# Performance work log

Hardware: AMD Instinct MI355X
Metric: run time of the kernel (lower is better)

Reference implementation:

```python
import jax, jax.numpy as jnp
import numpy as np

B = 512          # batch of visual features
VF_D = 4096      # visual feature dim (VGG fc7)
HID_D = 2048     # hidden dim
EMB_D = 300      # order-embedding / label-vector dim
N_LABELS = 2000  # number of GT label vectors


def setup_inputs() -> dict:
    key = jax.random.key(0)
    ks = jax.random.split(key, 4)
    vfs = jax.random.normal(ks[0], (B, VF_D), dtype=jnp.float32)
    W1 = jax.random.normal(ks[1], (VF_D, HID_D), dtype=jnp.float32) * (1.0 / np.sqrt(VF_D))
    b1 = jnp.zeros((HID_D,), dtype=jnp.float32)
    W2 = jax.random.normal(ks[2], (HID_D, EMB_D), dtype=jnp.float32) * (1.0 / np.sqrt(HID_D))
    b2 = jnp.zeros((EMB_D,), dtype=jnp.float32)
    gt_label_vecs = jax.random.normal(ks[3], (N_LABELS, EMB_D), dtype=jnp.float32)
    return {"vfs": vfs, "W1": W1, "b1": b1, "W2": W2, "b2": b2,
            "gt_label_vecs": gt_label_vecs}


def reference(vfs, W1, b1, W2, b2, gt_label_vecs):
    # hidden_layer: ReLU -> (Dropout, identity at eval) -> Linear
    vf_hidden = jnp.dot(jax.nn.relu(vfs), W1) + b1            # [B, HID_D]
    # embedding_layer: ReLU -> Linear
    vf_emb = jnp.dot(jax.nn.relu(vf_hidden), W2) + b2         # [B, EMB_D]
    # order_sim(hypers=gt_label_vecs, hypos=vf_emb):
    #   score = -|| clamp(hypo - hyper, min=0) ||^2, batched over all pairs
    diff = jax.nn.relu(vf_emb[:, None, :] - gt_label_vecs[None, :, :])  # [B, N, D]
    score_stack = -jnp.sum(diff * diff, axis=-1)              # [B, N_LABELS]
    return score_stack, vf_emb
```

## Files before the change

### kernel.cpp

```cpp
#include <hip/hip_runtime.h>

#define B_SZ   512
#define VFD    4096
#define HIDD   2048
#define EMBD   300
#define NLAB   2000
#define NPAD   320

#define G1_SPLIT 4
#define G2_SPLIT 8

typedef __attribute__((ext_vector_type(8))) short short8x;
typedef __attribute__((ext_vector_type(4))) float f32x4;
typedef __attribute__((ext_vector_type(8))) unsigned short ushort8;
typedef __attribute__((ext_vector_type(4))) unsigned short ushort4x;
typedef __attribute__((ext_vector_type(2))) _Float16 h2;

typedef const __attribute__((address_space(1))) unsigned int* gas_t;
typedef __attribute__((address_space(3))) unsigned int* las_t;

__device__ inline unsigned short f2bf(float x) {
    unsigned u = __float_as_uint(x);
    u += 0x7FFF + ((u >> 16) & 1);
    return (unsigned short)(u >> 16);
}

__device__ inline unsigned short f2hneg(float x) {
    _Float16 h = (_Float16)(-x);
    return __builtin_bit_cast(unsigned short, h);
}

__global__ __launch_bounds__(256) void prep_kernel(
    const float* __restrict__ vfs, unsigned short* __restrict__ Xb,
    const float* __restrict__ W1, unsigned short* __restrict__ W1T,
    const float* __restrict__ W2, unsigned short* __restrict__ W2T,
    const float* __restrict__ G,  unsigned short* __restrict__ Gh)
{
    __shared__ unsigned int Lds[64][34];
    const int tid = threadIdx.x;
    const int blk = blockIdx.x;

    if (blk < 1024) {
        const int i = (blk * 256 + tid) * 8;
        float4 a = *(const float4*)&vfs[i];
        float4 b = *(const float4*)&vfs[i + 4];
        ushort8 o;
        o[0] = f2bf(fmaxf(a.x, 0.f)); o[1] = f2bf(fmaxf(a.y, 0.f));
        o[2] = f2bf(fmaxf(a.z, 0.f)); o[3] = f2bf(fmaxf(a.w, 0.f));
        o[4] = f2bf(fmaxf(b.x, 0.f)); o[5] = f2bf(fmaxf(b.y, 0.f));
        o[6] = f2bf(fmaxf(b.z, 0.f)); o[7] = f2bf(fmaxf(b.w, 0.f));
        *(ushort8*)&Xb[i] = o;
        return;
    }
    if (blk >= 3232) {
        const int i = ((blk - 3232) * 256 + tid) * 8;
        if (i + 8 <= NLAB * EMBD) {
            float4 a = *(const float4*)&G[i];
            float4 b = *(const float4*)&G[i + 4];
            ushort8 o;
            o[0] = f2hneg(a.x); o[1] = f2hneg(a.y);
            o[2] = f2hneg(a.z); o[3] = f2hneg(a.w);
            o[4] = f2hneg(b.x); o[5] = f2hneg(b.y);
            o[6] = f2hneg(b.z); o[7] = f2hneg(b.w);
            *(ushort8*)&Gh[i] = o;
        }
        return;
    }

    const float* in; unsigned short* out; int N, ldK, bx, by;
    if (blk < 3072) {
        const int b = blk - 1024;
        in = W1; out = W1T; N = HIDD; ldK = VFD; bx = b & 31; by = b >> 5;
    } else {
        const int b = blk - 3072;
        in = W2; out = W2T; N = EMBD; ldK = HIDD; bx = b % 5; by = b / 5;
    }
    const int n0 = bx * 64, k0 = by * 64;

    #pragma unroll
    for (int i = 0; i < 2; ++i) {
        const int s = tid + 256 * i;
        const int kp = s >> 4, nq = s & 15;
        const int n = n0 + nq * 4;
        float4 v0 = {0.f,0.f,0.f,0.f}, v1 = {0.f,0.f,0.f,0.f};
        if (n < N) {
            v0 = *(const float4*)&in[(size_t)(k0 + 2 * kp)     * N + n];
            v1 = *(const float4*)&in[(size_t)(k0 + 2 * kp + 1) * N + n];
        }
        Lds[nq*4+0][kp] = (unsigned)f2bf(v0.x) | ((unsigned)f2bf(v1.x) << 16);
        Lds[nq*4+1][kp] = (unsigned)f2bf(v0.y) | ((unsigned)f2bf(v1.y) << 16);
        Lds[nq*4+2][kp] = (unsigned)f2bf(v0.z) | ((unsigned)f2bf(v1.z) << 16);
        Lds[nq*4+3][kp] = (unsigned)f2bf(v0.w) | ((unsigned)f2bf(v1.w) << 16);
    }
    __syncthreads();

    #pragma unroll
    for (int i = 0; i < 2; ++i) {
        const int c = tid + 256 * i;
        const int n = c >> 3, oct = c & 7;
        uint2 lo = *(uint2*)&Lds[n][oct * 4];
        uint2 hi = *(uint2*)&Lds[n][oct * 4 + 2];
        uint4 v = make_uint4(lo.x, lo.y, hi.x, hi.y);
        *(uint4*)&out[(size_t)(n0 + n) * ldK + k0 + oct * 8] = v;
    }
}

__global__ __launch_bounds__(256) void gemm1_kernel(
    const unsigned short* __restrict__ A,
    const unsigned short* __restrict__ Bt,
    float* __restrict__ Cpart)
{
    __shared__ unsigned short As[2][4096];
    __shared__ unsigned short Bs[2][8192];

    const int tid = threadIdx.x;
    const int m0 = blockIdx.y * 64, n0 = blockIdx.x * 128;
    const int kbase = blockIdx.z * (VFD / G1_SPLIT);

    const unsigned short* ga = A + (size_t)(m0 + (tid & 63)) * VFD + kbase + (tid >> 6) * 8;
    const unsigned short* gb = Bt + (size_t)(n0 + (tid & 127)) * VFD + kbase + (tid >> 7) * 8;

    const int lane = tid & 63;
    const int wave = tid >> 6;
    const int wm = (wave & 1) * 32;
    const int wn = (wave >> 1) * 64;
    const int q = lane >> 4, l15 = lane & 15;

    f32x4 acc[2][4];
    #pragma unroll
    for (int r = 0; r < 2; ++r)
        #pragma unroll
        for (int c = 0; c < 4; ++c) acc[r][c] = (f32x4){0.f,0.f,0.f,0.f};

    #pragma unroll
    for (int i = 0; i < 2; ++i)
        __builtin_amdgcn_global_load_lds((gas_t)(const void*)(ga + i * 32),
                                         (las_t)(void*)&As[0][(tid + 256 * i) * 8], 16, 0, 0);
    #pragma unroll
    for (int i = 0; i < 4; ++i)
        __builtin_amdgcn_global_load_lds((gas_t)(const void*)(gb + i * 16),
                                         (las_t)(void*)&Bs[0][(tid + 256 * i) * 8], 16, 0, 0);

    const int iters = (VFD / G1_SPLIT) / 64;
    for (int t = 0; t < iters; ++t) {
        const int cur = t & 1, nxt = cur ^ 1;
        __syncthreads();

        if (t + 1 < iters) {
            const int ko = (t + 1) * 64;
            #pragma unroll
            for (int i = 0; i < 2; ++i)
                __builtin_amdgcn_global_load_lds((gas_t)(const void*)(ga + ko + i * 32),
                                                 (las_t)(void*)&As[nxt][(tid + 256 * i) * 8], 16, 0, 0);
            #pragma unroll
            for (int i = 0; i < 4; ++i)
                __builtin_amdgcn_global_load_lds((gas_t)(const void*)(gb + ko + i * 16),
                                                 (las_t)(void*)&Bs[nxt][(tid + 256 * i) * 8], 16, 0, 0);
        }

        #pragma unroll
        for (int kk = 0; kk < 2; ++kk) {
            const int oct = kk * 4 + q;
            short8x a0 = *(short8x*)&As[cur][(oct * 64 + wm +      l15) * 8];
            short8x a1 = *(short8x*)&As[cur][(oct * 64 + wm + 16 + l15) * 8];
            #pragma unroll
            for (int c = 0; c < 4; ++c) {
                short8x b = *(short8x*)&Bs[cur][(oct * 128 + wn + c * 16 + l15) * 8];
                acc[0][c] = __builtin_amdgcn_mfma_f32_16x16x32_bf16(a0, b, acc[0][c], 0, 0, 0);
                acc[1][c] = __builtin_amdgcn_mfma_f32_16x16x32_bf16(a1, b, acc[1][c], 0, 0, 0);
            }
        }
    }

    float* Cz = Cpart + (size_t)blockIdx.z * B_SZ * HIDD;
    #pragma unroll
    for (int r = 0; r < 2; ++r) {
        #pragma unroll
        for (int g = 0; g < 4; ++g) {
            const int rr = m0 + wm + r * 16 + q * 4 + g;
            #pragma unroll
            for (int c = 0; c < 4; ++c)
                Cz[(size_t)rr * HIDD + n0 + wn + c * 16 + l15] = acc[r][c][g];
        }
    }
}

template<int LDA, int LDB, int LDC, int KCHUNK>
__global__ __launch_bounds__(256) void gemm_bf16_kernel(
    const unsigned short* __restrict__ A,
    const unsigned short* __restrict__ Bt,
    float* __restrict__ Cpart, int M)
{
    __shared__ unsigned short As[2][4096];
    __shared__ unsigned short Bs[2][4096];

    const int tid = threadIdx.x;
    const int m0 = blockIdx.y * 64, n0 = blockIdx.x * 64;
    const int kbase = blockIdx.z * KCHUNK;

    const unsigned short* ga = A  + (size_t)(m0 + (tid & 63)) * LDA + kbase + (tid >> 6) * 8;
    const unsigned short* gb = Bt + (size_t)(n0 + (tid & 63)) * LDB + kbase + (tid >> 6) * 8;

    const int lane = tid & 63;
    const int wave = tid >> 6;
    const int wm = (wave & 1) * 32;
    const int wn = (wave >> 1) * 32;
    const int q = lane >> 4, l15 = lane & 15;

    f32x4 acc00 = {0.f,0.f,0.f,0.f}, acc01 = {0.f,0.f,0.f,0.f};
    f32x4 acc10 = {0.f,0.f,0.f,0.f}, acc11 = {0.f,0.f,0.f,0.f};

    #pragma unroll
    for (int i = 0; i < 2; ++i) {
        __builtin_amdgcn_global_load_lds((gas_t)(const void*)(ga + i * 32),
                                         (las_t)(void*)&As[0][(tid + 256 * i) * 8], 16, 0, 0);
        __builtin_amdgcn_global_load_lds((gas_t)(const void*)(gb + i * 32),
                                         (las_t)(void*)&Bs[0][(tid + 256 * i) * 8], 16, 0, 0);
    }

    const int iters = KCHUNK / 64;
    for (int t = 0; t < iters; ++t) {
        const int cur = t & 1, nxt = cur ^ 1;
        __syncthreads();

        if (t + 1 < iters) {
            const int ko = (t + 1) * 64;
            #pragma unroll
            for (int i = 0; i < 2; ++i) {
                __builtin_amdgcn_global_load_lds((gas_t)(const void*)(ga + ko + i * 32),
                                                 (las_t)(void*)&As[nxt][(tid + 256 * i) * 8], 16, 0, 0);
                __builtin_amdgcn_global_load_lds((gas_t)(const void*)(gb + ko + i * 32),
                                                 (las_t)(void*)&Bs[nxt][(tid + 256 * i) * 8], 16, 0, 0);
            }
        }

        #pragma unroll
        for (int kk = 0; kk < 2; ++kk) {
            const int oct = kk * 4 + q;
            short8x a0 = *(short8x*)&As[cur][(oct * 64 + wm +      l15) * 8];
            short8x a1 = *(short8x*)&As[cur][(oct * 64 + wm + 16 + l15) * 8];
            short8x b0 = *(short8x*)&Bs[cur][(oct * 64 + wn +      l15) * 8];
            short8x b1 = *(short8x*)&Bs[cur][(oct * 64 + wn + 16 + l15) * 8];
            acc00 = __builtin_amdgcn_mfma_f32_16x16x32_bf16(a0, b0, acc00, 0, 0, 0);
            acc01 = __builtin_amdgcn_mfma_f32_16x16x32_bf16(a0, b1, acc01, 0, 0, 0);
            acc10 = __builtin_amdgcn_mfma_f32_16x16x32_bf16(a1, b0, acc10, 0, 0, 0);
            acc11 = __builtin_amdgcn_mfma_f32_16x16x32_bf16(a1, b1, acc11, 0, 0, 0);
        }
    }

    float* Cz = Cpart + (size_t)blockIdx.z * M * LDC;
    #pragma unroll
    for (int r = 0; r < 4; ++r) {
        const int rr = m0 + wm + q * 4 + r;
        const int cc = n0 + wn + l15;
        Cz[(size_t)rr * LDC + cc]             = acc00[r];
        Cz[(size_t)rr * LDC + cc + 16]        = acc01[r];
        Cz[(size_t)(rr + 16) * LDC + cc]      = acc10[r];
        Cz[(size_t)(rr + 16) * LDC + cc + 16] = acc11[r];
    }
}

__global__ __launch_bounds__(256) void reduce_h_kernel(
    const float* __restrict__ Hpart, const float* __restrict__ b1,
    unsigned short* __restrict__ Hb)
{
    const int i = (blockIdx.x * 256 + threadIdx.x) * 4;
    const int col = i & (HIDD - 1);
    float4 s = *(const float4*)&b1[col];
    #pragma unroll
    for (int z = 0; z < G1_SPLIT; ++z) {
        float4 p = *(const float4*)&Hpart[(size_t)z * B_SZ * HIDD + i];
        s.x += p.x; s.y += p.y; s.z += p.z; s.w += p.w;
    }
    ushort4x o;
    o[0] = f2bf(fmaxf(s.x, 0.f));
    o[1] = f2bf(fmaxf(s.y, 0.f));
    o[2] = f2bf(fmaxf(s.z, 0.f));
    o[3] = f2bf(fmaxf(s.w, 0.f));
    *(ushort4x*)&Hb[i] = o;
}

__global__ __launch_bounds__(256) void reduce_e_kernel(
    const float* __restrict__ Epart, const float* __restrict__ b2,
    float* __restrict__ E, unsigned short* __restrict__ Eh)
{
    const int gid = blockIdx.x * 256 + threadIdx.x;
    if (gid >= B_SZ * EMBD) return;
    const int m = gid / EMBD, n = gid - m * EMBD;
    float v = b2[n];
    #pragma unroll
    for (int z = 0; z < G2_SPLIT; ++z)
        v += Epart[(size_t)z * B_SZ * NPAD + m * NPAD + n];
    E[gid] = v;
    Eh[gid] = __builtin_bit_cast(unsigned short, (_Float16)v);
}

__global__ __launch_bounds__(256) void scores_kernel(
    const unsigned short* __restrict__ Eh,
    const unsigned short* __restrict__ Gh,
    float* __restrict__ scores)
{
    __shared__ unsigned short Gs[64][44];

    const int tid = threadIdx.x;
    const int tx = tid & 15, ty = tid >> 4;
    const int n0 = blockIdx.x * 64, b0 = blockIdx.y * 32;

    const h2 hz = {(_Float16)0.0f, (_Float16)0.0f};
    float acc[2][4] = {};

    for (int d0 = 0; d0 < NPAD; d0 += 40) {
        __syncthreads();
        #pragma unroll
        for (int i = 0; i < 3; ++i) {
            const int s = tid + 256 * i;
            if (s < 640) {
                const int row = s / 10, qd = (s - row * 10) * 4;
                const int n = n0 + row, d = d0 + qd;
                uint2 v = make_uint2(0u, 0u);
                if (n < NLAB && d < EMBD) v = *(const uint2*)&Gh[(size_t)n * EMBD + d];
                *(uint2*)&Gs[row][qd] = v;
            }
        }
        __syncthreads();

        #pragma unroll
        for (int d = 0; d < 40; d += 4) {
            const int dd = d0 + d;
            h2 e0[2], e1[2];
            #pragma unroll
            for (int r = 0; r < 2; ++r) {
                uint2 ev = make_uint2(0u, 0u);
                if (dd < EMBD)
                    ev = *(const uint2*)&Eh[(size_t)(b0 + ty * 2 + r) * EMBD + dd];
                e0[r] = __builtin_bit_cast(h2, ev.x);
                e1[r] = __builtin_bit_cast(h2, ev.y);
            }
            #pragma unroll
            for (int c = 0; c < 4; ++c) {
                uint2 gv = *(const uint2*)&Gs[tx + 16 * c][d];
                const h2 g0 = __builtin_bit_cast(h2, gv.x);
                const h2 g1 = __builtin_bit_cast(h2, gv.y);
                #pragma unroll
                for (int r = 0; r < 2; ++r) {
                    h2 s0 = e0[r] + g0;
                    h2 s1 = e1[r] + g1;
                    s0 = __builtin_elementwise_max(s0, hz);
                    s1 = __builtin_elementwise_max(s1, hz);
                    acc[r][c] = __builtin_amdgcn_fdot2(s0, s0, acc[r][c], false);
                    acc[r][c] = __builtin_amdgcn_fdot2(s1, s1, acc[r][c], false);
                }
            }
        }
    }

    #pragma unroll
    for (int r = 0; r < 2; ++r) {
        const int b = b0 + ty * 2 + r;
        #pragma unroll
        for (int c = 0; c < 4; ++c) {
            const int n = n0 + tx + 16 * c;
            if (n < NLAB) scores[(size_t)b * NLAB + n] = -acc[r][c];
        }
    }
}

extern "C" void kernel_launch(void* const* d_in, const int* in_sizes, int n_in,
                              void* d_out, int out_size, void* d_ws, size_t ws_size,
                              hipStream_t stream)
{
    const float* vfs = (const float*)d_in[0];
    const float* W1  = (const float*)d_in[1];
    const float* b1  = (const float*)d_in[2];
    const float* W2  = (const float*)d_in[3];
    const float* b2  = (const float*)d_in[4];
    const float* G   = (const float*)d_in[5];

    float* out    = (float*)d_out;
    float* scores = out;
    float* E      = out + (size_t)B_SZ * NLAB;

    char* ws = (char*)d_ws;
    unsigned short* Xb  = (unsigned short*)(ws);
    unsigned short* W1T = (unsigned short*)(ws + 4194304);
    unsigned short* W2T = (unsigned short*)(ws + 20971520);
    unsigned short* Hb  = (unsigned short*)(ws + 22282240);
    float*          Hpart = (float*)(ws + 24379392);
    float*          Epart = (float*)(ws + 41156608);
    unsigned short* Gh  = (unsigned short*)(ws + 46399488);
    unsigned short* Eh  = (unsigned short*)(ws + 47599488);

    prep_kernel<<<3525, 256, 0, stream>>>(vfs, Xb, W1, W1T, W2, W2T, G, Gh);

    gemm1_kernel<<<dim3(16, 8, G1_SPLIT), 256, 0, stream>>>(Xb, W1T, Hpart);
    reduce_h_kernel<<<1024, 256, 0, stream>>>(Hpart, b1, Hb);

    gemm_bf16_kernel<HIDD, HIDD, NPAD, HIDD / G2_SPLIT>
        <<<dim3(5, 8, G2_SPLIT), 256, 0, stream>>>(Hb, W2T, Epart, B_SZ);
    reduce_e_kernel<<<600, 256, 0, stream>>>(Epart, b2, E, Eh);

    scores_kernel<<<dim3(32, 16), 256, 0, stream>>>(Eh, Gh, scores);
}
```

Baseline: 161.5 us.

## Store split-K partials as bf16, fuse E reduction via atomics, drop reduce_e

GEMM1 split-K partials are now written as bf16 instead of fp32, which halves the write and read traffic through reduce_h. GEMM2 accumulates directly into E with atomicAdd, after E is pre-initialised with b2 in the prep kernel. This removes the Epart buffer and the reduce_e launch. The scores kernel reads fp32 E and converts it to fp16 on the fly with pkrtz, using 60-wide d chunks with no padding. The risks are bf16 rounding of partial sums, nondeterministic atomic ordering, and atomic contention across 8 K-splits.

Result: slower. 168.5 us (+4.3%).

```diff
diff --git a/kernel.cpp b/kernel.cpp
--- a/kernel.cpp
+++ b/kernel.cpp
@@ -5,7 +5,6 @@
 #define HIDD   2048
 #define EMBD   300
 #define NLAB   2000
-#define NPAD   320
 
 #define G1_SPLIT 4
 #define G2_SPLIT 8
@@ -13,7 +12,6 @@
 typedef __attribute__((ext_vector_type(8))) short short8x;
 typedef __attribute__((ext_vector_type(4))) float f32x4;
 typedef __attribute__((ext_vector_type(8))) unsigned short ushort8;
-typedef __attribute__((ext_vector_type(4))) unsigned short ushort4x;
 typedef __attribute__((ext_vector_type(2))) _Float16 h2;
 
 typedef const __attribute__((address_space(1))) unsigned int* gas_t;
@@ -30,11 +28,16 @@
     return __builtin_bit_cast(unsigned short, h);
 }
 
+__device__ inline h2 pkrtz(float a, float b) {
+    return __builtin_bit_cast(h2, __builtin_amdgcn_cvt_pkrtz(a, b));
+}
+
 __global__ __launch_bounds__(256) void prep_kernel(
     const float* __restrict__ vfs, unsigned short* __restrict__ Xb,
     const float* __restrict__ W1, unsigned short* __restrict__ W1T,
     const float* __restrict__ W2, unsigned short* __restrict__ W2T,
-    const float* __restrict__ G,  unsigned short* __restrict__ Gh)
+    const float* __restrict__ G,  unsigned short* __restrict__ Gh,
+    const float* __restrict__ b2, float* __restrict__ E)
 {
     __shared__ unsigned int Lds[64][34];
     const int tid = threadIdx.x;
@@ -52,6 +55,13 @@
         *(ushort8*)&Xb[i] = o;
         return;
     }
+    if (blk >= 3525) {
+        const int i = ((blk - 3525) * 256 + tid) * 4;
+        const int n = i % EMBD;
+        float4 bv = *(const float4*)&b2[n];
+        *(float4*)&E[i] = bv;
+        return;
+    }
     if (blk >= 3232) {
         const int i = ((blk - 3232) * 256 + tid) * 8;
         if (i + 8 <= NLAB * EMBD) {
@@ -108,7 +118,7 @@
 __global__ __launch_bounds__(256) void gemm1_kernel(
     const unsigned short* __restrict__ A,
     const unsigned short* __restrict__ Bt,
-    float* __restrict__ Cpart)
+    unsigned short* __restrict__ Cpart)
 {
     __shared__ unsigned short As[2][4096];
     __shared__ unsigned short Bs[2][8192];
@@ -172,7 +182,7 @@
         }
     }
 
-    float* Cz = Cpart + (size_t)blockIdx.z * B_SZ * HIDD;
+    unsigned short* Cz = Cpart + (size_t)blockIdx.z * B_SZ * HIDD;
     #pragma unroll
     for (int r = 0; r < 2; ++r) {
         #pragma unroll
@@ -180,26 +190,25 @@
             const int rr = m0 + wm + r * 16 + q * 4 + g;
             #pragma unroll
             for (int c = 0; c < 4; ++c)
-                Cz[(size_t)rr * HIDD + n0 + wn + c * 16 + l15] = acc[r][c][g];
-        }
-    }
-}
-
-template<int LDA, int LDB, int LDC, int KCHUNK>
-__global__ __launch_bounds__(256) void gemm_bf16_kernel(
+                Cz[(size_t)rr * HIDD + n0 + wn + c * 16 + l15] = f2bf(acc[r][c][g]);
+        }
+    }
+}
+
+__global__ __launch_bounds__(256) void gemm2_kernel(
     const unsigned short* __restrict__ A,
     const unsigned short* __restrict__ Bt,
-    float* __restrict__ Cpart, int M)
+    float* __restrict__ E)
 {
     __shared__ unsigned short As[2][4096];
     __shared__ unsigned short Bs[2][4096];
 
     const int tid = threadIdx.x;
     const int m0 = blockIdx.y * 64, n0 = blockIdx.x * 64;
-    const int kbase = blockIdx.z * KCHUNK;
-
-    const unsigned short* ga = A  + (size_t)(m0 + (tid & 63)) * LDA + kbase + (tid >> 6) * 8;
-    const unsigned short* gb = Bt + (size_t)(n0 + (tid & 63)) * LDB + kbase + (tid >> 6) * 8;
+    const int kbase = blockIdx.z * (HIDD / G2_SPLIT);
+
+    const unsigned short* ga = A  + (size_t)(m0 + (tid & 63)) * HIDD + kbase + (tid >> 6) * 8;
+    const unsigned short* gb = Bt + (size_t)(n0 + (tid & 63)) * HIDD + kbase + (tid >> 6) * 8;
 
     const int lane = tid & 63;
     const int wave = tid >> 6;
@@ -218,7 +227,7 @@
                                          (las_t)(void*)&Bs[0][(tid + 256 * i) * 8], 16, 0, 0);
     }
 
-    const int iters = KCHUNK / 64;
+    const int iters = (HIDD / G2_SPLIT) / 64;
     for (int t = 0; t < iters; ++t) {
         const int cur = t & 1, nxt = cur ^ 1;
         __syncthreads();
@@ -248,59 +257,51 @@
         }
     }
 
-    float* Cz = Cpart + (size_t)blockIdx.z * M * LDC;
     #pragma unroll
     for (int r = 0; r < 4; ++r) {
         const int rr = m0 + wm + q * 4 + r;
         const int cc = n0 + wn + l15;
-        Cz[(size_t)rr * LDC + cc]             = acc00[r];
-        Cz[(size_t)rr * LDC + cc + 16]        = acc01[r];
-        Cz[(size_t)(rr + 16) * LDC + cc]      = acc10[r];
-        Cz[(size_t)(rr + 16) * LDC + cc + 16] = acc11[r];
+        if (cc < EMBD) {
+            atomicAdd(&E[(size_t)rr * EMBD + cc],        acc00[r]);
+            atomicAdd(&E[(size_t)(rr + 16) * EMBD + cc], acc10[r]);
+        }
+        if (cc + 16 < EMBD) {
+            atomicAdd(&E[(size_t)rr * EMBD + cc + 16],        acc01[r]);
+            atomicAdd(&E[(size_t)(rr + 16) * EMBD + cc + 16], acc11[r]);
+        }
     }
 }
 
 __global__ __launch_bounds__(256) void reduce_h_kernel(
-    const float* __restrict__ Hpart, const float* __restrict__ b1,
+    const unsigned short* __restrict__ Hpart, const float* __restrict__ b1,
     unsigned short* __restrict__ Hb)
 {
-    const int i = (blockIdx.x * 256 + threadIdx.x) * 4;
+    const int i = (blockIdx.x * 256 + threadIdx.x) * 8;
     const int col = i & (HIDD - 1);
-    float4 s = *(const float4*)&b1[col];
+    float s[8];
+    float4 ba = *(const float4*)&b1[col];
+    float4 bb = *(const float4*)&b1[col + 4];
+    s[0]=ba.x; s[1]=ba.y; s[2]=ba.z; s[3]=ba.w;
+    s[4]=bb.x; s[5]=bb.y; s[6]=bb.z; s[7]=bb.w;
     #pragma unroll
     for (int z = 0; z < G1_SPLIT; ++z) {
-        float4 p = *(const float4*)&Hpart[(size_t)z * B_SZ * HIDD + i];
-        s.x += p.x; s.y += p.y; s.z += p.z; s.w += p.w;
-    }
-    ushort4x o;
-    o[0] = f2bf(fmaxf(s.x, 0.f));
-    o[1] = f2bf(fmaxf(s.y, 0.f));
-    o[2] = f2bf(fmaxf(s.z, 0.f));
-    o[3] = f2bf(fmaxf(s.w, 0.f));
-    *(ushort4x*)&Hb[i] = o;
-}
-
-__global__ __launch_bounds__(256) void reduce_e_kernel(
-    const float* __restrict__ Epart, const float* __restrict__ b2,
-    float* __restrict__ E, unsigned short* __restrict__ Eh)
-{
-    const int gid = blockIdx.x * 256 + threadIdx.x;
-    if (gid >= B_SZ * EMBD) return;
-    const int m = gid / EMBD, n = gid - m * EMBD;
-    float v = b2[n];
-    #pragma unroll
-    for (int z = 0; z < G2_SPLIT; ++z)
-        v += Epart[(size_t)z * B_SZ * NPAD + m * NPAD + n];
-    E[gid] = v;
-    Eh[gid] = __builtin_bit_cast(unsigned short, (_Float16)v);
+        ushort8 p = *(const ushort8*)&Hpart[(size_t)z * B_SZ * HIDD + i];
+        #pragma unroll
+        for (int j = 0; j < 8; ++j)
+            s[j] += __uint_as_float((unsigned)p[j] << 16);
+    }
+    ushort8 o;
+    #pragma unroll
+    for (int j = 0; j < 8; ++j) o[j] = f2bf(fmaxf(s[j], 0.f));
+    *(ushort8*)&Hb[i] = o;
 }
 
 __global__ __launch_bounds__(256) void scores_kernel(
-    const unsigned short* __restrict__ Eh,
+    const float* __restrict__ E,
     const unsigned short* __restrict__ Gh,
     float* __restrict__ scores)
 {
-    __shared__ unsigned short Gs[64][44];
+    __shared__ unsigned short Gs[64][60];
 
     const int tid = threadIdx.x;
     const int tx = tid & 15, ty = tid >> 4;
@@ -309,32 +310,30 @@
     const h2 hz = {(_Float16)0.0f, (_Float16)0.0f};
     float acc[2][4] = {};
 
-    for (int d0 = 0; d0 < NPAD; d0 += 40) {
+    for (int d0 = 0; d0 < EMBD; d0 += 60) {
         __syncthreads();
         #pragma unroll
-        for (int i = 0; i < 3; ++i) {
+        for (int i = 0; i < 4; ++i) {
             const int s = tid + 256 * i;
-            if (s < 640) {
-                const int row = s / 10, qd = (s - row * 10) * 4;
-                const int n = n0 + row, d = d0 + qd;
+            if (s < 960) {
+                const int row = s / 15, qd = (s - row * 15) * 4;
+                const int n = n0 + row;
                 uint2 v = make_uint2(0u, 0u);
-                if (n < NLAB && d < EMBD) v = *(const uint2*)&Gh[(size_t)n * EMBD + d];
+                if (n < NLAB) v = *(const uint2*)&Gh[(size_t)n * EMBD + d0 + qd];
                 *(uint2*)&Gs[row][qd] = v;
             }
         }
         __syncthreads();
 
         #pragma unroll
-        for (int d = 0; d < 40; d += 4) {
+        for (int d = 0; d < 60; d += 4) {
             const int dd = d0 + d;
             h2 e0[2], e1[2];
             #pragma unroll
             for (int r = 0; r < 2; ++r) {
-                uint2 ev = make_uint2(0u, 0u);
-                if (dd < EMBD)
-                    ev = *(const uint2*)&Eh[(size_t)(b0 + ty * 2 + r) * EMBD + dd];
-                e0[r] = __builtin_bit_cast(h2, ev.x);
-                e1[r] = __builtin_bit_cast(h2, ev.y);
+                float4 ev = *(const float4*)&E[(size_t)(b0 + ty * 2 + r) * EMBD + dd];
+                e0[r] = pkrtz(ev.x, ev.y);
+                e1[r] = pkrtz(ev.z, ev.w);
             }
             #pragma unroll
             for (int c = 0; c < 4; ++c) {
@@ -385,19 +384,15 @@
     unsigned short* W1T = (unsigned short*)(ws + 4194304);
     unsigned short* W2T = (unsigned short*)(ws + 20971520);
     unsigned short* Hb  = (unsigned short*)(ws + 22282240);
-    float*          Hpart = (float*)(ws + 24379392);
-    float*          Epart = (float*)(ws + 41156608);
-    unsigned short* Gh  = (unsigned short*)(ws + 46399488);
-    unsigned short* Eh  = (unsigned short*)(ws + 47599488);
-
-    prep_kernel<<<3525, 256, 0, stream>>>(vfs, Xb, W1, W1T, W2, W2T, G, Gh);
+    unsigned short* Hpart = (unsigned short*)(ws + 24379392);
+    unsigned short* Gh  = (unsigned short*)(ws + 32768000);
+
+    prep_kernel<<<3675, 256, 0, stream>>>(vfs, Xb, W1, W1T, W2, W2T, G, Gh, b2, E);
 
     gemm1_kernel<<<dim3(16, 8, G1_SPLIT), 256, 0, stream>>>(Xb, W1T, Hpart);
-    reduce_h_kernel<<<1024, 256, 0, stream>>>(Hpart, b1, Hb);
-
-    gemm_bf16_kernel<HIDD, HIDD, NPAD, HIDD / G2_SPLIT>
-        <<<dim3(5, 8, G2_SPLIT), 256, 0, stream>>>(Hb, W2T, Epart, B_SZ);
-    reduce_e_kernel<<<600, 256, 0, stream>>>(Epart, b2, E, Eh);
-
-    scores_kernel<<<dim3(32, 16), 256, 0, stream>>>(Eh, Gh, scores);
-}
+    reduce_h_kernel<<<512, 256, 0, stream>>>(Hpart, b1, Hb);
+
+    gemm2_kernel<<<dim3(5, 8, G2_SPLIT), 256, 0, stream>>>(Hb, W2T, E);
+
+    scores_kernel<<<dim3(32, 16), 256, 0, stream>>>(E, Gh, scores);
+}
```
